# Kernel tuning notes

Measured on AMD Instinct MI355X. Metric: run time of the kernel, lower is better.

The kernel has to match this reference:

```python
import jax, jax.numpy as jnp
import numpy as np

B, P, K, E, H, V, C = 128, 64, 64, 300, 300, 50000, 3


def lstm0(x, Wih, bih, bhh):
    # PyTorch LSTMCell single step with zero initial (h, c) state.
    # gates = x @ Wih^T + bih + Whh @ 0 + bhh ; chunks order: i, f, g, o
    g = x @ Wih.T + bih + bhh
    i, f, gg, o = jnp.split(g, 4, axis=-1)
    c = jax.nn.sigmoid(i) * jnp.tanh(gg)
    return jax.nn.sigmoid(o) * jnp.tanh(c)


def setup_inputs() -> dict:
    key = jax.random.key(0)
    ks = jax.random.split(key, 24)
    d = {}
    d["premise"] = jax.random.randint(ks[0], (B, P), 1, V)
    d["premise_len"] = jax.random.randint(ks[1], (B,), P // 2, P + 1)
    d["hypothesis"] = jax.random.randint(ks[2], (B, K), 1, V)
    d["hypothesis_len"] = jax.random.randint(ks[3], (B,), K // 2, K + 1)
    embed = jax.random.normal(ks[4], (V, E), jnp.float32) * 0.1
    d["embed"] = embed.at[0].set(0.0)  # padding_idx=0
    d["w_e"] = jax.random.uniform(ks[5], (H,), jnp.float32)
    xav = (2.0 / (H + H)) ** 0.5
    d["W_s"] = jax.random.normal(ks[6], (H, H), jnp.float32) * xav
    d["W_t"] = jax.random.normal(ks[7], (H, H), jnp.float32) * xav
    d["W_m"] = jax.random.normal(ks[8], (H, H), jnp.float32) * xav
    d["fc_w"] = jax.random.normal(ks[9], (C, H), jnp.float32) * (2.0 / (H + C)) ** 0.5
    d["fc_b"] = jax.random.uniform(ks[10], (C,), jnp.float32)
    s = 1.0 / np.sqrt(H)
    def cell(k1, k2, k3, k4, in_dim):
        return (jax.random.uniform(k1, (4 * H, in_dim), jnp.float32, -s, s),
                jax.random.uniform(k2, (4 * H, H), jnp.float32, -s, s),
                jax.random.uniform(k3, (4 * H,), jnp.float32, -s, s),
                jax.random.uniform(k4, (4 * H,), jnp.float32, -s, s))
    d["Wih_p"], d["Whh_p"], d["bih_p"], d["bhh_p"] = cell(ks[11], ks[12], ks[13], ks[14], E)
    d["Wih_h"], d["Whh_h"], d["bih_h"], d["bhh_h"] = cell(ks[15], ks[16], ks[17], ks[18], E)
    d["Wih_m"], d["Whh_m"], d["bih_m"], d["bhh_m"] = cell(ks[19], ks[20], ks[21], ks[22], 2 * H)
    return d


def reference(premise, premise_len, hypothesis, hypothesis_len, embed, w_e,
              W_s, W_t, W_m, fc_w, fc_b,
              Wih_p, Whh_p, bih_p, bhh_p,
              Wih_h, Whh_h, bih_h, bhh_h,
              Wih_m, Whh_m, bih_m, bhh_m):
    prem_emb = embed[premise]      # [B,P,E]
    hypo_emb = embed[hypothesis]   # [B,K,E]
    # Original code calls LSTMCell on a whole sequence -> per-token single step
    # with zero initial state (no temporal recurrence in these two cells).
    h_s = lstm0(prem_emb, Wih_p, bih_p, bhh_p)  # [B,P,H]
    h_t = lstm0(hypo_emb, Wih_h, bih_h, bhh_h)  # [B,K,H]
    s_proj = h_s @ W_s.T                         # [B,P,H]
    t_proj = jnp.transpose(h_t @ W_t.T, (1, 0, 2))  # [K,B,H]
    h_t_kb = jnp.transpose(h_t, (1, 0, 2))          # [K,B,H]
    b, p = h_s.shape[0], h_s.shape[1]
    pmask = jnp.arange(p)[None, :] < premise_len[:, None]  # [B,P]
    neg = jnp.finfo(s_proj.dtype).min

    def step(h_m, xs):
        t_k, ht_k = xs  # [B,H], [B,H]
        m_proj = h_m @ W_m.T  # [B,H]
        e = jnp.einsum('bph,h->bp',
                       jnp.tanh(s_proj + t_k[:, None, :] + m_proj[:, None, :]), w_e)
        e = jnp.where(pmask, e, neg)
        alpha = jax.nn.softmax(e, axis=1)           # softmax over valid premise pos
        a = jnp.einsum('bp,bph->bh', alpha, h_s)    # attention-weighted premise
        m = jnp.concatenate([a, ht_k], axis=-1)     # [B,2H]
        # lstm_match is re-invoked with zero state each k in the original
        h_m_new = lstm0(m, Wih_m, bih_m, bhh_m)
        return h_m_new, h_m_new

    _, hs_all = jax.lax.scan(step, jnp.zeros((b, s_proj.shape[-1]), s_proj.dtype),
                             (t_proj, h_t_kb))      # [K,B,H]
    h_fin = hs_all[hypothesis_len - 1, jnp.arange(b)]  # h_m at last valid hypo step
    logits = h_fin @ fc_w.T + fc_b
    return jax.nn.softmax(logits, axis=1)
```

## Files before the change

### kernel.cpp

```cpp
#include <hip/hip_runtime.h>
#include <stdint.h>

typedef unsigned short u16;
typedef __attribute__((ext_vector_type(8))) __bf16 bf16x8;
typedef __attribute__((ext_vector_type(4))) float f32x4;

__device__ __forceinline__ float bf2f(u16 u) {
    union { unsigned int i; float f; } v; v.i = ((unsigned int)u) << 16; return v.f;
}
__device__ __forceinline__ float bf2f_lo(unsigned int u) {
    union { unsigned int i; float f; } v; v.i = u << 16; return v.f;
}
__device__ __forceinline__ float bf2f_hi(unsigned int u) {
    union { unsigned int i; float f; } v; v.i = u & 0xffff0000u; return v.f;
}
__device__ __forceinline__ u16 f2bf(float f) {
    union { float f; unsigned int i; } v; v.f = f;
    unsigned int x = v.i;
    unsigned int r = (x + 0x7fffu + ((x >> 16) & 1u)) >> 16;
    return (u16)r;
}
__device__ __forceinline__ float rdf(const void* p, size_t i, int isbf) {
    return isbf ? bf2f(((const u16*)p)[i]) : ((const float*)p)[i];
}
__device__ __forceinline__ float fast_sigmoid(float x) {
    return __builtin_amdgcn_rcpf(1.f + __expf(-x));
}
__device__ __forceinline__ float fast_tanh(float x) {
    float u = __expf(x + x);
    return 1.f - 2.f * __builtin_amdgcn_rcpf(u + 1.f);
}
__device__ __forceinline__ bf16x8 as_bf8(uint4 u) {
    union { uint4 a; bf16x8 b; } c; c.a = u; return c.b;
}

#define BB 128
#define PP 64
#define KK 64
#define HH 300
#define MROWS 8192
#define KPAD 320
#define N3H 900
#define GLD 912
#define NT1 19
#define NT4 57

__global__ void detect_dtype(const u16* __restrict__ raw, int* __restrict__ flag) {
    __shared__ int cnt;
    if (threadIdx.x == 0) cnt = 0;
    __syncthreads();
    if (threadIdx.x < 300 && (raw[threadIdx.x] & 0x8000u)) atomicAdd(&cnt, 1);
    __syncthreads();
    if (threadIdx.x == 0) *flag = (cnt < 8) ? 1 : 0;
}

__global__ void pack_w(const void* __restrict__ src, u16* __restrict__ dst,
                       int dstRowsPad, int nsrcRows, int srcld, int colOff, int igo,
                       const int* __restrict__ flag) {
    int i = blockIdx.x * 256 + threadIdx.x;
    if (i >= dstRowsPad * KPAD) return;
    int isbf = *flag;
    int r = i / KPAD, c = i % KPAD;
    u16 v = 0;
    if (r < nsrcRows && c < HH) {
        int sr = igo ? (r < HH ? r : r + HH) : r;
        v = f2bf(rdf(src, (size_t)sr * srcld + colOff + c, isbf));
    }
    dst[i] = v;
}

__global__ void pack_wf(const void* __restrict__ Wm, uint4* __restrict__ dst,
                        const int* __restrict__ flag) {
    int i = blockIdx.x * 256 + threadIdx.x;
    if (i >= NT1 * 10 * 64) return;
    int isbf = *flag;
    int lane = i & 63, ks = (i >> 6) % 10, T = i / 640;
    int j = T * 16 + (lane & 15);
    int k0 = 32 * ks + 8 * (lane >> 4);
    unsigned int d[4];
    #pragma unroll
    for (int q = 0; q < 4; ++q) {
        int ka = k0 + 2 * q, kb = k0 + 2 * q + 1;
        unsigned int lo = (j < 300 && ka < 300) ? f2bf(rdf(Wm, (size_t)j * HH + ka, isbf)) : 0;
        unsigned int hi = (j < 300 && kb < 300) ? f2bf(rdf(Wm, (size_t)j * HH + kb, isbf)) : 0;
        d[q] = lo | (hi << 16);
    }
    uint4 v; v.x = d[0]; v.y = d[1]; v.z = d[2]; v.w = d[3];
    dst[i] = v;
}

__global__ void pack_bias(const void* bip, const void* bhp, const void* bih_, const void* bhh_,
                          const void* bim, const void* bhm,
                          float* bp, float* bh, float* bm, const int* __restrict__ flag) {
    int i = blockIdx.x * 256 + threadIdx.x;
    if (i >= 3 * N3H) return;
    int isbf = *flag;
    int which = i / N3H, r = i % N3H;
    int sr = (r < HH) ? r : r + HH;
    if (which == 0)      bp[r] = rdf(bip, sr, isbf) + rdf(bhp, sr, isbf);
    else if (which == 1) bh[r] = rdf(bih_, sr, isbf) + rdf(bhh_, sr, isbf);
    else                 bm[r] = rdf(bim, sr, isbf) + rdf(bhm, sr, isbf);
}

__global__ void gather_embed(const int* __restrict__ idx, const void* __restrict__ embed,
                             u16* __restrict__ X, const int* __restrict__ flag) {
    int i = blockIdx.x * 256 + threadIdx.x;
    int isbf = *flag;
    int r = i / KPAD, c = i % KPAD;
    X[i] = (c < HH) ? f2bf(rdf(embed, (size_t)idx[r] * HH + c, isbf)) : (u16)0;
}

__global__ void zero_out(u16* out) { out[threadIdx.x] = 0; }

__global__ __launch_bounds__(256) void gemm_bt(
    const u16* __restrict__ A, const u16* __restrict__ B,
    u16* __restrict__ Cb, const float* __restrict__ bias, int N, int ldc, int frag)
{
    __shared__ __align__(16) u16 At[128 * 32];
    __shared__ __align__(16) u16 Bt[128 * 32];
    const int tid = threadIdx.x;
    const int m0 = blockIdx.x * 128;
    const int n0 = blockIdx.y * 128;
    const int lane = tid & 63;
    const int wave = tid >> 6;
    const int rm = (wave & 1) * 64;
    const int rn = (wave >> 1) * 64;
    const int qr = lane >> 4;
    const int lr = lane & 15;

    f32x4 acc[4][4] = {};

    const int c0 = tid, c1 = tid + 256;
    const int r0 = c0 >> 2, o0 = (c0 & 3) * 8;
    const int r1 = c1 >> 2, o1 = (c1 & 3) * 8;

    for (int k0 = 0; k0 < KPAD; k0 += 32) {
        uint4 a0v = *(const uint4*)(A + (size_t)(m0 + r0) * KPAD + k0 + o0);
        uint4 a1v = *(const uint4*)(A + (size_t)(m0 + r1) * KPAD + k0 + o1);
        uint4 b0v = *(const uint4*)(B + (size_t)(n0 + r0) * KPAD + k0 + o0);
        uint4 b1v = *(const uint4*)(B + (size_t)(n0 + r1) * KPAD + k0 + o1);
        __syncthreads();
        *(uint4*)(At + c0 * 8) = a0v;
        *(uint4*)(At + c1 * 8) = a1v;
        *(uint4*)(Bt + c0 * 8) = b0v;
        *(uint4*)(Bt + c1 * 8) = b1v;
        __syncthreads();
        bf16x8 af[4], bfr[4];
        #pragma unroll
        for (int i = 0; i < 4; ++i) {
            af[i]  = *(const bf16x8*)(At + (rm + i * 16 + lr) * 32 + qr * 8);
            bfr[i] = *(const bf16x8*)(Bt + (rn + i * 16 + lr) * 32 + qr * 8);
        }
        #pragma unroll
        for (int mi = 0; mi < 4; ++mi)
            #pragma unroll
            for (int ni = 0; ni < 4; ++ni)
                acc[mi][ni] = __builtin_amdgcn_mfma_f32_16x16x32_bf16(
                    af[mi], bfr[ni], acc[mi][ni], 0, 0, 0);
    }
    #pragma unroll
    for (int mi = 0; mi < 4; ++mi) {
        #pragma unroll
        for (int ni = 0; ni < 4; ++ni) {
            int n = n0 + rn + ni * 16 + lr;
            int mb = m0 + rm + mi * 16 + qr * 4;
            if (!frag) {
                if (n >= ldc) continue;
                if (n < N) {
                    float bv = bias ? bias[n] : 0.f;
                    #pragma unroll
                    for (int r = 0; r < 4; ++r)
                        Cb[(size_t)(mb + r) * ldc + n] = f2bf(acc[mi][ni][r] + bv);
                } else {
                    #pragma unroll
                    for (int r = 0; r < 4; ++r)
                        Cb[(size_t)(mb + r) * ldc + n] = 0;
                }
            } else {
                if (n >= GLD) continue;
                int bb = mb >> 6, p0 = mb & 63;
                size_t base = ((((size_t)bb * NT4 + (n >> 4)) * 2 + (p0 >> 5)) * 64
                               + ((p0 >> 3) & 3) * 16 + (n & 15)) * 8 + (p0 & 7);
                u16 wv[4];
                if (n < N) {
                    float bv = bias ? bias[n] : 0.f;
                    #pragma unroll
                    for (int r = 0; r < 4; ++r) wv[r] = f2bf(acc[mi][ni][r] + bv);
                } else {
                    #pragma unroll
                    for (int r = 0; r < 4; ++r) wv[r] = 0;
                }
                uint2 st;
                st.x = (unsigned int)wv[0] | ((unsigned int)wv[1] << 16);
                st.y = (unsigned int)wv[2] | ((unsigned int)wv[3] << 16);
                *(uint2*)(Cb + base) = st;
            }
        }
    }
}

__global__ void lstm_act(const u16* __restrict__ gates, u16* __restrict__ hout) {
    int idx = blockIdx.x * 256 + threadIdx.x;
    int r = idx / KPAD, c = idx % KPAD;
    float h = 0.f;
    if (c < HH) {
        const u16* g = gates + (size_t)r * N3H;
        float gi = bf2f(g[c]);
        float gg = bf2f(g[c + HH]);
        float go = bf2f(g[c + 2 * HH]);
        float cc = fast_sigmoid(gi) * fast_tanh(gg);
        h = fast_sigmoid(go) * fast_tanh(cc);
    }
    hout[idx] = f2bf(h);
}

__global__ __launch_bounds__(512, 1) void scan_kernel(
    const u16* __restrict__ sproj,
    const u16* __restrict__ tproj,
    const uint4* __restrict__ Gmf,
    const u16* __restrict__ hp,
    const uint4* __restrict__ Wf,
    const void* __restrict__ w_e,
    const int* __restrict__ premise_len,
    const int* __restrict__ hypothesis_len,
    float* __restrict__ hfin,
    const int* __restrict__ flag)
{
    __shared__ __align__(16) uint4 wlds[3 * 10 * 64];
    __shared__ __align__(16) float we2[320];
    __shared__ __align__(16) float tpm[320];
    __shared__ __align__(16) unsigned int hmhi[160];
    __shared__ __align__(16) unsigned int hmlo[160];
    __shared__ __align__(16) u16 aw[8][128];
    __shared__ float evals[64];
    __shared__ __align__(16) float gates[912];

    const int b = blockIdx.x, t = threadIdx.x;
    const int lane = t & 63, w = t >> 6;
    const int lr = lane & 15, qr = lane >> 4;
    const int plen = premise_len[b], hlen = hypothesis_len[b];
    const int isbf = *flag;

    for (int i = t; i < 3 * 10 * 64; i += 512) wlds[i] = Wf[16 * 640 + i];
    if (t < 320) { we2[t] = (t < 300) ? 2.f * rdf(w_e, t, isbf) : 0.f; tpm[t] = 0.f; }
    if (t < 160) { hmhi[t] = 0; hmlo[t] = 0; }

    uint4 wreg[20];
    #pragma unroll
    for (int ks = 0; ks < 10; ++ks) wreg[ks]      = Wf[(size_t)w * 640 + ks * 64 + lane];
    #pragma unroll
    for (int ks = 0; ks < 10; ++ks) wreg[10 + ks] = Wf[(size_t)(w + 8) * 640 + ks * 64 + lane];

    const int nt4 = (w == 0) ? 8 : 7;
    uint4 greg[16];
    {
        const uint4* gsrc = Gmf + (size_t)b * (NT4 * 2 * 64);
        #pragma unroll
        for (int i = 0; i < 8; ++i) {
            if (i < nt4) {
                int T = w + 8 * i;
                greg[2 * i]     = gsrc[(T * 2 + 0) * 64 + lane];
                greg[2 * i + 1] = gsrc[(T * 2 + 1) * 64 + lane];
            }
        }
    }

    const int p2p = t >> 3, p2s = t & 7;
    unsigned int spd[20];
    {
        const uint4* sprow = (const uint4*)(sproj + (size_t)(b * PP + p2p) * KPAD + 40 * p2s);
        #pragma unroll
        for (int q = 0; q < 5; ++q) {
            uint4 v = sprow[q];
            spd[4 * q] = v.x; spd[4 * q + 1] = v.y; spd[4 * q + 2] = v.z; spd[4 * q + 3] = v.w;
        }
    }
    __syncthreads();

    float wsum = 0.f;
    #pragma unroll
    for (int q = 0; q < 10; ++q) {
        float4 v = ((const float4*)we2)[10 * p2s + q];
        wsum += 0.5f * ((v.x + v.y) + (v.z + v.w));
    }

    for (int k = 0; k < hlen; ++k) {
        const u16* tprow = tproj + (size_t)(b * KK + k) * KPAD;
        const u16* hprow = hp + (size_t)(b * KK + k) * 900;

        u16 hpv[8];
        #pragma unroll
        for (int i = 0; i < 8; ++i) {
            hpv[i] = 0;
            if (i < nt4 && lane < 16) hpv[i] = hprow[(w + 8 * i) * 16 + lane];
        }
        u16 tk0 = 0, tk1 = 0, tk2 = 0;
        if (lane < 16) {
            tk0 = tprow[w * 16 + lane];
            tk1 = tprow[(w + 8) * 16 + lane];
            if (w < 3) tk2 = tprow[(w + 16) * 16 + lane];
        }

        bf16x8 a1[10];
        {
            const unsigned int* abase = (lr == 1) ? hmlo : hmhi;
            uint4 z; z.x = 0; z.y = 0; z.z = 0; z.w = 0;
            #pragma unroll
            for (int ks = 0; ks < 10; ++ks) {
                uint4 u = *(const uint4*)(abase + 16 * ks + 4 * qr);
                a1[ks] = as_bf8((lr < 2) ? u : z);
            }
        }
        {
            f32x4 ac0 = {}, ac1 = {};
            #pragma unroll
            for (int ks = 0; ks < 10; ks += 2) {
                ac0 = __builtin_amdgcn_mfma_f32_16x16x32_bf16(a1[ks], as_bf8(wreg[ks]), ac0, 0, 0, 0);
                ac1 = __builtin_amdgcn_mfma_f32_16x16x32_bf16(a1[ks + 1], as_bf8(wreg[ks + 1]), ac1, 0, 0, 0);
            }
            if (lane < 16) tpm[w * 16 + lane] = 2.f * (bf2f(tk0) + ((ac0[0] + ac0[1]) + (ac1[0] + ac1[1])));
        }
        {
            f32x4 ac0 = {}, ac1 = {};
            #pragma unroll
            for (int ks = 0; ks < 10; ks += 2) {
                ac0 = __builtin_amdgcn_mfma_f32_16x16x32_bf16(a1[ks], as_bf8(wreg[10 + ks]), ac0, 0, 0, 0);
                ac1 = __builtin_amdgcn_mfma_f32_16x16x32_bf16(a1[ks + 1], as_bf8(wreg[11 + ks]), ac1, 0, 0, 0);
            }
            if (lane < 16) tpm[(w + 8) * 16 + lane] = 2.f * (bf2f(tk1) + ((ac0[0] + ac0[1]) + (ac1[0] + ac1[1])));
        }
        if (w < 3) {
            f32x4 ac0 = {}, ac1 = {};
            #pragma unroll
            for (int ks = 0; ks < 10; ks += 2) {
                bf16x8 b0 = as_bf8(wlds[w * 640 + ks * 64 + lane]);
                bf16x8 b1 = as_bf8(wlds[w * 640 + (ks + 1) * 64 + lane]);
                ac0 = __builtin_amdgcn_mfma_f32_16x16x32_bf16(a1[ks], b0, ac0, 0, 0, 0);
                ac1 = __builtin_amdgcn_mfma_f32_16x16x32_bf16(a1[ks + 1], b1, ac1, 0, 0, 0);
            }
            if (lane < 16) tpm[(w + 16) * 16 + lane] = 2.f * (bf2f(tk2) + ((ac0[0] + ac0[1]) + (ac1[0] + ac1[1])));
        }
        __syncthreads();

        {
            float accn = 0.f;
            bool act = p2p < plen;
            if (act) {
                #pragma unroll
                for (int q = 0; q < 10; ++q) {
                    float4 tv = ((const float4*)tpm)[10 * p2s + q];
                    float4 wv = ((const float4*)we2)[10 * p2s + q];
                    float x0 = fmaf(2.f, bf2f_lo(spd[2 * q]), tv.x);
                    float x1 = fmaf(2.f, bf2f_hi(spd[2 * q]), tv.y);
                    float x2 = fmaf(2.f, bf2f_lo(spd[2 * q + 1]), tv.z);
                    float x3 = fmaf(2.f, bf2f_hi(spd[2 * q + 1]), tv.w);
                    accn = fmaf(wv.x, __builtin_amdgcn_rcpf(__expf(x0) + 1.f), accn);
                    accn = fmaf(wv.y, __builtin_amdgcn_rcpf(__expf(x1) + 1.f), accn);
                    accn = fmaf(wv.z, __builtin_amdgcn_rcpf(__expf(x2) + 1.f), accn);
                    accn = fmaf(wv.w, __builtin_amdgcn_rcpf(__expf(x3) + 1.f), accn);
                }
            }
            float val = act ? (wsum - accn) : 0.f;
            val += __shfl_down(val, 4);
            val += __shfl_down(val, 2);
            val += __shfl_down(val, 1);
            if (p2s == 0) evals[p2p] = act ? val : -1e30f;
        }
        __syncthreads();

        {
            float v = evals[lane];
            float mx = v;
            #pragma unroll
            for (int d = 32; d; d >>= 1) mx = fmaxf(mx, __shfl_xor(mx, d));
            float ex = (lane < plen) ? __expf(v - mx) : 0.f;
            float sm = ex;
            #pragma unroll
            for (int d = 32; d; d >>= 1) sm += __shfl_xor(sm, d);
            float al = ex * __builtin_amdgcn_rcpf(sm);
            u16 ah = f2bf(al);
            aw[w][lane] = ah;
            aw[w][64 + lane] = f2bf(al - bf2f(ah));
        }

        bf16x8 a4[2];
        {
            const u16* abase = aw[w] + ((lr == 1) ? 64 : 0);
            uint4 z; z.x = 0; z.y = 0; z.z = 0; z.w = 0;
            #pragma unroll
            for (int ks = 0; ks < 2; ++ks) {
                uint4 u = *(const uint4*)(abase + 32 * ks + 8 * qr);
                a4[ks] = as_bf8((lr < 2) ? u : z);
            }
        }
        #pragma unroll
        for (int i = 0; i < 8; ++i) {
            if (i < nt4) {
                int T = w + 8 * i;
                f32x4 ac0 = {}, ac1 = {};
                ac0 = __builtin_amdgcn_mfma_f32_16x16x32_bf16(a4[0], as_bf8(greg[2 * i]), ac0, 0, 0, 0);
                ac1 = __builtin_amdgcn_mfma_f32_16x16x32_bf16(a4[1], as_bf8(greg[2 * i + 1]), ac1, 0, 0, 0);
                if (lane < 16) gates[T * 16 + lane] = ((ac0[0] + ac0[1]) + (ac1[0] + ac1[1])) + bf2f(hpv[i]);
            }
        }
        __syncthreads();

        if (t < 300) {
            float gi = gates[t], gg = gates[300 + t], go = gates[600 + t];
            float cc = fast_sigmoid(gi) * fast_tanh(gg);
            float h = fast_sigmoid(go) * fast_tanh(cc);
            if (k == hlen - 1) hfin[(size_t)b * KPAD + t] = h;
            u16 hh = f2bf(h);
            float res = h - bf2f(hh);
            float hn = __shfl_down(h, 1);
            float rn2 = __shfl_down(res, 1);
            if ((t & 1) == 0) {
                hmhi[t >> 1] = (unsigned int)hh | ((unsigned int)f2bf(hn) << 16);
                hmlo[t >> 1] = (unsigned int)f2bf(res) | ((unsigned int)f2bf(rn2) << 16);
            }
        }
        __syncthreads();
    }
}

__global__ void fc_softmax(const float* __restrict__ hfin, const void* __restrict__ fcw,
                           const void* __restrict__ fcb, void* __restrict__ out,
                           const int* __restrict__ flag) {
    int b = threadIdx.x;
    int isbf = *flag;
    float l[3];
    #pragma unroll
    for (int c = 0; c < 3; ++c) {
        float acc = rdf(fcb, c, isbf);
        const float* hr = hfin + (size_t)b * KPAD;
        for (int h = 0; h < HH; ++h) acc += hr[h] * rdf(fcw, (size_t)c * HH + h, isbf);
        l[c] = acc;
    }
    float mx = fmaxf(l[0], fmaxf(l[1], l[2]));
    float e0 = __expf(l[0] - mx), e1 = __expf(l[1] - mx), e2 = __expf(l[2] - mx);
    float inv = __builtin_amdgcn_rcpf(e0 + e1 + e2);
    if (isbf) {
        u16* o = (u16*)out;
        o[b * 3 + 0] = f2bf(e0 * inv);
        o[b * 3 + 1] = f2bf(e1 * inv);
        o[b * 3 + 2] = f2bf(e2 * inv);
    } else {
        float* o = (float*)out;
        o[b * 3 + 0] = e0 * inv;
        o[b * 3 + 1] = e1 * inv;
        o[b * 3 + 2] = e2 * inv;
    }
}

extern "C" void kernel_launch(void* const* d_in, const int* in_sizes, int n_in,
                              void* d_out, int out_size, void* d_ws, size_t ws_size,
                              hipStream_t stream) {
    const int* premise        = (const int*)d_in[0];
    const int* premise_len    = (const int*)d_in[1];
    const int* hypothesis     = (const int*)d_in[2];
    const int* hypothesis_len = (const int*)d_in[3];
    const void* embed = d_in[4];
    const void* w_e   = d_in[5];
    const void* W_s   = d_in[6];
    const void* W_t   = d_in[7];
    const void* W_m   = d_in[8];
    const void* fc_w  = d_in[9];
    const void* fc_b  = d_in[10];
    const void* Wih_p = d_in[11];
    const void* bih_p = d_in[13];
    const void* bhh_p = d_in[14];
    const void* Wih_h = d_in[15];
    const void* bih_h = d_in[17];
    const void* bhh_h = d_in[18];
    const void* Wih_m = d_in[19];
    const void* bih_m = d_in[21];
    const void* bhh_m = d_in[22];
    (void)in_sizes; (void)n_in; (void)out_size;

    char* w = (char*)d_ws;
    auto alloc = [&](size_t bytes) -> char* {
        char* r = (char*)(((uintptr_t)w + 255) & ~(uintptr_t)255);
        w = r + bytes;
        return r;
    };
    char* regA = alloc((size_t)MROWS * KPAD * 2);
    char* regB = alloc((size_t)MROWS * GLD * 2);
    char* regC = alloc((size_t)MROWS * N3H * 2);
    char* regD = alloc((size_t)MROWS * KPAD * 2);
    char* regE = alloc((size_t)MROWS * KPAD * 2);
    u16* Wp_pad  = (u16*)alloc((size_t)1024 * KPAD * 2);
    u16* Wh_pad  = (u16*)alloc((size_t)1024 * KPAD * 2);
    u16* Wa_pad  = (u16*)alloc((size_t)1024 * KPAD * 2);
    u16* Whm_pad = (u16*)alloc((size_t)1024 * KPAD * 2);
    u16* Ws_pad  = (u16*)alloc((size_t)384 * KPAD * 2);
    u16* Wt_pad  = (u16*)alloc((size_t)384 * KPAD * 2);
    uint4* Wf    = (uint4*)alloc((size_t)NT1 * 10 * 64 * 16);
    float* bsum_p = (float*)alloc(N3H * 4);
    float* bsum_h = (float*)alloc(N3H * 4);
    float* bsum_m = (float*)alloc(N3H * 4);
    int* dflag   = (int*)alloc(256);
    size_t needed = (size_t)(w - (char*)d_ws);
    if (needed > ws_size) {
        zero_out<<<1, 384, 0, stream>>>((u16*)d_out);
        return;
    }
    u16* Xbuf   = (u16*)regA;
    u16* s_proj = (u16*)regA;
    u16* h_s    = (u16*)regD;
    u16* t_proj = (u16*)regD;
    u16* h_t    = (u16*)regE;
    float* h_fin = (float*)regE;

    detect_dtype<<<1, 320, 0, stream>>>((const u16*)w_e, dflag);
    pack_w<<<1280, 256, 0, stream>>>(Wih_p, Wp_pad, 1024, N3H, HH, 0, 1, dflag);
    pack_w<<<1280, 256, 0, stream>>>(Wih_h, Wh_pad, 1024, N3H, HH, 0, 1, dflag);
    pack_w<<<1280, 256, 0, stream>>>(Wih_m, Wa_pad, 1024, N3H, 600, 0, 1, dflag);
    pack_w<<<1280, 256, 0, stream>>>(Wih_m, Whm_pad, 1024, N3H, 600, HH, 1, dflag);
    pack_w<<<480, 256, 0, stream>>>(W_s, Ws_pad, 384, HH, HH, 0, 0, dflag);
    pack_w<<<480, 256, 0, stream>>>(W_t, Wt_pad, 384, HH, HH, 0, 0, dflag);
    pack_wf<<<48, 256, 0, stream>>>(W_m, Wf, dflag);
    pack_bias<<<11, 256, 0, stream>>>(bih_p, bhh_p, bih_h, bhh_h, bih_m, bhh_m,
                                      bsum_p, bsum_h, bsum_m, dflag);

    gather_embed<<<10240, 256, 0, stream>>>(premise, embed, Xbuf, dflag);
    gemm_bt<<<dim3(64, 8), 256, 0, stream>>>(Xbuf, Wp_pad, (u16*)regB, bsum_p, N3H, N3H, 0);
    lstm_act<<<10240, 256, 0, stream>>>((u16*)regB, h_s);
    gather_embed<<<10240, 256, 0, stream>>>(hypothesis, embed, Xbuf, dflag);
    gemm_bt<<<dim3(64, 8), 256, 0, stream>>>(Xbuf, Wh_pad, (u16*)regC, bsum_h, N3H, N3H, 0);
    lstm_act<<<10240, 256, 0, stream>>>((u16*)regC, h_t);

    gemm_bt<<<dim3(64, 3), 256, 0, stream>>>(h_s, Ws_pad, s_proj, nullptr, HH, KPAD, 0);
    gemm_bt<<<dim3(64, 8), 256, 0, stream>>>(h_s, Wa_pad, (u16*)regB, nullptr, N3H, 0, 1);
    gemm_bt<<<dim3(64, 3), 256, 0, stream>>>(h_t, Wt_pad, t_proj, nullptr, HH, KPAD, 0);
    gemm_bt<<<dim3(64, 8), 256, 0, stream>>>(h_t, Whm_pad, (u16*)regC, bsum_m, N3H, N3H, 0);

    scan_kernel<<<BB, 512, 0, stream>>>(s_proj, t_proj, (const uint4*)regB,
                                        (const u16*)regC, Wf, w_e,
                                        premise_len, hypothesis_len, h_fin, dflag);
    fc_softmax<<<1, 128, 0, stream>>>(h_fin, fc_w, fc_b, d_out, dflag);
}
```

Measured before the change: 688.8 us.

## Move per-batch gate weights to LDS and target two waves per EU

The per-batch Gmf weight fragments are now staged once into shared memory instead of living in 64 VGPRs per thread. The launch attribute moves from one block per CU to amdgpu_waves_per_eu(2,2), which caps register use so two blocks can share a CU. The two register-weight MFMA chains are also interleaved into four independent accumulators to raise instruction-level parallelism. The trade is extra LDS traffic on every step and higher LDS use per block, which may limit whether two blocks actually fit.

```diff
diff --git a/kernel.cpp b/kernel.cpp
--- a/kernel.cpp
+++ b/kernel.cpp
@@ -214,7 +214,9 @@
     hout[idx] = f2bf(h);
 }
 
-__global__ __launch_bounds__(512, 1) void scan_kernel(
+__global__ __launch_bounds__(512)
+__attribute__((amdgpu_waves_per_eu(2, 2)))
+void scan_kernel(
     const u16* __restrict__ sproj,
     const u16* __restrict__ tproj,
     const uint4* __restrict__ Gmf,
@@ -226,6 +228,7 @@
     float* __restrict__ hfin,
     const int* __restrict__ flag)
 {
+    __shared__ __align__(16) uint4 gml[NT4 * 2 * 64];
     __shared__ __align__(16) uint4 wlds[3 * 10 * 64];
     __shared__ __align__(16) float we2[320];
     __shared__ __align__(16) float tpm[320];
@@ -242,6 +245,10 @@
     const int isbf = *flag;
 
     for (int i = t; i < 3 * 10 * 64; i += 512) wlds[i] = Wf[16 * 640 + i];
+    {
+        const uint4* gsrc = Gmf + (size_t)b * (NT4 * 2 * 64);
+        for (int i = t; i < NT4 * 2 * 64; i += 512) gml[i] = gsrc[i];
+    }
     if (t < 320) { we2[t] = (t < 300) ? 2.f * rdf(w_e, t, isbf) : 0.f; tpm[t] = 0.f; }
     if (t < 160) { hmhi[t] = 0; hmlo[t] = 0; }
 
@@ -250,20 +257,6 @@
     for (int ks = 0; ks < 10; ++ks) wreg[ks]      = Wf[(size_t)w * 640 + ks * 64 + lane];
     #pragma unroll
     for (int ks = 0; ks < 10; ++ks) wreg[10 + ks] = Wf[(size_t)(w + 8) * 640 + ks * 64 + lane];
-
-    const int nt4 = (w == 0) ? 8 : 7;
-    uint4 greg[16];
-    {
-        const uint4* gsrc = Gmf + (size_t)b * (NT4 * 2 * 64);
-        #pragma unroll
-        for (int i = 0; i < 8; ++i) {
-            if (i < nt4) {
-                int T = w + 8 * i;
-                greg[2 * i]     = gsrc[(T * 2 + 0) * 64 + lane];
-                greg[2 * i + 1] = gsrc[(T * 2 + 1) * 64 + lane];
-            }
-        }
-    }
 
     const int p2p = t >> 3, p2s = t & 7;
     unsigned int spd[20];
@@ -284,6 +277,8 @@
         wsum += 0.5f * ((v.x + v.y) + (v.z + v.w));
     }
 
+    const int nt4 = (w == 0) ? 8 : 7;
+
     for (int k = 0; k < hlen; ++k) {
         const u16* tprow = tproj + (size_t)(b * KK + k) * KPAD;
         const u16* hprow = hp + (size_t)(b * KK + k) * 900;
@@ -312,22 +307,18 @@
             }
         }
         {
-            f32x4 ac0 = {}, ac1 = {};
+            f32x4 aW0 = {}, aW1 = {}, aV0 = {}, aV1 = {};
             #pragma unroll
             for (int ks = 0; ks < 10; ks += 2) {
-                ac0 = __builtin_amdgcn_mfma_f32_16x16x32_bf16(a1[ks], as_bf8(wreg[ks]), ac0, 0, 0, 0);
-                ac1 = __builtin_amdgcn_mfma_f32_16x16x32_bf16(a1[ks + 1], as_bf8(wreg[ks + 1]), ac1, 0, 0, 0);
-            }
-            if (lane < 16) tpm[w * 16 + lane] = 2.f * (bf2f(tk0) + ((ac0[0] + ac0[1]) + (ac1[0] + ac1[1])));
-        }
-        {
-            f32x4 ac0 = {}, ac1 = {};
-            #pragma unroll
-            for (int ks = 0; ks < 10; ks += 2) {
-                ac0 = __builtin_amdgcn_mfma_f32_16x16x32_bf16(a1[ks], as_bf8(wreg[10 + ks]), ac0, 0, 0, 0);
-                ac1 = __builtin_amdgcn_mfma_f32_16x16x32_bf16(a1[ks + 1], as_bf8(wreg[11 + ks]), ac1, 0, 0, 0);
-            }
-            if (lane < 16) tpm[(w + 8) * 16 + lane] = 2.f * (bf2f(tk1) + ((ac0[0] + ac0[1]) + (ac1[0] + ac1[1])));
+                aW0 = __builtin_amdgcn_mfma_f32_16x16x32_bf16(a1[ks], as_bf8(wreg[ks]), aW0, 0, 0, 0);
+                aV0 = __builtin_amdgcn_mfma_f32_16x16x32_bf16(a1[ks], as_bf8(wreg[10 + ks]), aV0, 0, 0, 0);
+                aW1 = __builtin_amdgcn_mfma_f32_16x16x32_bf16(a1[ks + 1], as_bf8(wreg[ks + 1]), aW1, 0, 0, 0);
+                aV1 = __builtin_amdgcn_mfma_f32_16x16x32_bf16(a1[ks + 1], as_bf8(wreg[11 + ks]), aV1, 0, 0, 0);
+            }
+            if (lane < 16) {
+                tpm[w * 16 + lane]       = 2.f * (bf2f(tk0) + ((aW0[0] + aW0[1]) + (aW1[0] + aW1[1])));
+                tpm[(w + 8) * 16 + lane] = 2.f * (bf2f(tk1) + ((aV0[0] + aV0[1]) + (aV1[0] + aV1[1])));
+            }
         }
         if (w < 3) {
             f32x4 ac0 = {}, ac1 = {};
@@ -398,8 +389,8 @@
             if (i < nt4) {
                 int T = w + 8 * i;
                 f32x4 ac0 = {}, ac1 = {};
-                ac0 = __builtin_amdgcn_mfma_f32_16x16x32_bf16(a4[0], as_bf8(greg[2 * i]), ac0, 0, 0, 0);
-                ac1 = __builtin_amdgcn_mfma_f32_16x16x32_bf16(a4[1], as_bf8(greg[2 * i + 1]), ac1, 0, 0, 0);
+                ac0 = __builtin_amdgcn_mfma_f32_16x16x32_bf16(a4[0], as_bf8(gml[(T * 2 + 0) * 64 + lane]), ac0, 0, 0, 0);
+                ac1 = __builtin_amdgcn_mfma_f32_16x16x32_bf16(a4[1], as_bf8(gml[(T * 2 + 1) * 64 + lane]), ac1, 0, 0, 0);
                 if (lane < 16) gates[T * 16 + lane] = ((ac0[0] + ac0[1]) + (ac1[0] + ac1[1])) + bf2f(hpv[i]);
             }
         }
```

Result: faster. 672.0 us (-2.4%).
